# Optimization experiments

Measured on AMD Instinct MI355X. Metric: run time of the kernel, lower is better.

## Reference

```python
import jax, jax.numpy as jnp
import numpy as np

VOCAB = 1000
PAD_ID = 0
D = 256      # d_model
H = 256      # hidden_size
G = 4 * H    # LSTM gate width
B = 64
S = 256      # src_len
TGT = 257    # tgt_len (decode T = 256)


def setup_inputs() -> dict:
    key = jax.random.key(0)
    ks = iter(jax.random.split(key, 48))
    def p(shape, scale):
        return jax.random.normal(next(ks), shape, jnp.float32) * scale
    inp = {}
    inp['src'] = jax.random.randint(next(ks), (B, S), 1, VOCAB)    # no PAD tokens
    inp['tgt'] = jax.random.randint(next(ks), (B, TGT), 1, VOCAB)
    inp['emb'] = p((VOCAB, D), D ** -0.5).at[PAD_ID].set(0.0)       # padding_idx row zeroed
    s = 1.0 / np.sqrt(H)
    # encoder biLSTM: layer0 fwd/bwd (input D), layer1 fwd/bwd (input 2H)
    for name, din in [('e0f', D), ('e0b', D), ('e1f', 2 * H), ('e1b', 2 * H)]:
        inp[name + '_Wih'] = p((G, din), 1.0 / np.sqrt(din))
        inp[name + '_Whh'] = p((G, H), s)
        inp[name + '_bih'] = p((G,), s)
        inp[name + '_bhh'] = p((G,), s)
    # decoder LSTM: layer0 input D+2H, layer1 input H
    for name, din in [('d0', D + 2 * H), ('d1', H)]:
        inp[name + '_Wih'] = p((G, din), 1.0 / np.sqrt(din))
        inp[name + '_Whh'] = p((G, H), s)
        inp[name + '_bih'] = p((G,), s)
        inp[name + '_bhh'] = p((G,), s)
    inp['h_proj_W'] = p((H, 2 * H), 1.0 / np.sqrt(2 * H))
    inp['h_proj_b'] = p((H,), s)
    inp['c_proj_W'] = p((H, 2 * H), 1.0 / np.sqrt(2 * H))
    inp['c_proj_b'] = p((H,), s)
    inp['att_Wenc'] = p((H, 2 * H), 1.0 / np.sqrt(2 * H))
    inp['att_Wdec'] = p((H, H), s)
    inp['att_v'] = p((H,), s)
    return inp


def _cell(gates, c):
    # PyTorch gate order: i, f, g, o
    i, f, g, o = jnp.split(gates, 4, axis=-1)
    c = jax.nn.sigmoid(f) * c + jax.nn.sigmoid(i) * jnp.tanh(g)
    return jax.nn.sigmoid(o) * jnp.tanh(c), c


def _lstm(x, Wih, Whh, bih, bhh, reverse=False):
    # x: (B, S, din) -> outputs (B, S, H), final (h, c)
    Bsz = x.shape[0]
    Hd = Whh.shape[1]
    pre = jnp.swapaxes(x @ Wih.T + bih + bhh, 0, 1)  # (S, B, 4H)
    def step(carry, g):
        h, c = carry
        h, c = _cell(g + h @ Whh.T, c)
        return (h, c), h
    init = (jnp.zeros((Bsz, Hd), x.dtype), jnp.zeros((Bsz, Hd), x.dtype))
    (hT, cT), ys = jax.lax.scan(step, init, pre, reverse=reverse)
    return jnp.swapaxes(ys, 0, 1), hT, cT


def reference(src, tgt, emb,
              e0f_Wih, e0f_Whh, e0f_bih, e0f_bhh,
              e0b_Wih, e0b_Whh, e0b_bih, e0b_bhh,
              e1f_Wih, e1f_Whh, e1f_bih, e1f_bhh,
              e1b_Wih, e1b_Whh, e1b_bih, e1b_bhh,
              d0_Wih, d0_Whh, d0_bih, d0_bhh,
              d1_Wih, d1_Whh, d1_bih, d1_bhh,
              h_proj_W, h_proj_b, c_proj_W, c_proj_b,
              att_Wenc, att_Wdec, att_v):
    mask = (src == PAD_ID)                       # (B, S), all False here
    x0 = emb[src]                                # (B, S, D)
    # ---- bidirectional 2-layer encoder ----
    f0, _, _ = _lstm(x0, e0f_Wih, e0f_Whh, e0f_bih, e0f_bhh)
    b0, _, _ = _lstm(x0, e0b_Wih, e0b_Whh, e0b_bih, e0b_bhh, reverse=True)
    x1 = jnp.concatenate([f0, b0], axis=-1)      # (B, S, 2H)
    f1, hf, cf = _lstm(x1, e1f_Wih, e1f_Whh, e1f_bih, e1f_bhh)
    b1, hb, cb = _lstm(x1, e1b_Wih, e1b_Whh, e1b_bih, e1b_bhh, reverse=True)
    enc_out = jnp.concatenate([f1, b1], axis=-1)  # (B, S, 2H)
    # ---- decoder init (shared across both decoder layers) ----
    h0 = jnp.tanh(jnp.concatenate([hf, hb], -1) @ h_proj_W.T + h_proj_b)
    c0 = jnp.tanh(jnp.concatenate([cf, cb], -1) @ c_proj_W.T + c_proj_b)
    # ---- teacher-forced decode with Bahdanau attention ----
    enc_proj = enc_out @ att_Wenc.T              # (B, S, H), hoisted out of the loop
    tgt_emb = emb[tgt[:, :-1]]                   # (B, T, D)

    def dec_step(carry, xt):
        hl0, cl0, hl1, cl1 = carry
        energy = jnp.tanh(enc_proj + (hl1 @ att_Wdec.T)[:, None, :])  # (B, S, H)
        scores = energy @ att_v                                        # (B, S)
        scores = jnp.where(mask, -jnp.inf, scores)
        w = jax.nn.softmax(scores, axis=-1)
        ctx = jnp.einsum('bs,bse->be', w, enc_out)                     # (B, 2H)
        x = jnp.concatenate([xt, ctx], axis=-1)                        # (B, D+2H)
        hl0, cl0 = _cell(x @ d0_Wih.T + d0_bih + d0_bhh + hl0 @ d0_Whh.T, cl0)
        hl1, cl1 = _cell(hl0 @ d1_Wih.T + d1_bih + d1_bhh + hl1 @ d1_Whh.T, cl1)
        return (hl0, cl0, hl1, cl1), hl1

    _, outs = jax.lax.scan(dec_step, (h0, c0, h0, c0), jnp.swapaxes(tgt_emb, 0, 1))
    out = jnp.swapaxes(outs, 0, 1)               # (B, T, H); out_proj is None (H == D)
    return out @ emb.T                           # weight-tied fc_out -> (B, T, VOCAB)
```

## Files before the change

### kernel.cpp

```cpp
#include <hip/hip_runtime.h>
#include <hip/hip_bf16.h>
#include <stdint.h>

#define B_ 64
#define S_ 256
#define T_ 256
#define D_ 256
#define H_ 256
#define V_ 1000

__device__ __forceinline__ float blo(unsigned u){ return __uint_as_float(u << 16); }
__device__ __forceinline__ float bhi(unsigned u){ return __uint_as_float(u & 0xffff0000u); }
__device__ __forceinline__ float sigm(float x){ return 1.0f / (1.0f + __expf(-x)); }
__device__ __forceinline__ float tanhfast(float x){ float e = __expf(2.0f * x); return 1.0f - 2.0f / (e + 1.0f); }

__device__ __forceinline__ void cellupd(float a0, float a1, float a2, float a3, float& c, float& h){
  float cn = sigm(a1) * c + sigm(a0) * tanhfast(a2);
  c = cn;
  h = sigm(a3) * tanhfast(cn);
}

__device__ __forceinline__ float wredmax(float v){
  #pragma unroll
  for (int o = 32; o > 0; o >>= 1) v = fmaxf(v, __shfl_xor(v, o));
  return v;
}
__device__ __forceinline__ float wredsum(float v){
  #pragma unroll
  for (int o = 32; o > 0; o >>= 1) v += __shfl_xor(v, o);
  return v;
}

__device__ __forceinline__ void ast(float* p, float v){
  __hip_atomic_store(p, v, __ATOMIC_RELAXED, __HIP_MEMORY_SCOPE_AGENT);
}
__device__ __forceinline__ float ald(const float* p){
  return __hip_atomic_load(p, __ATOMIC_RELAXED, __HIP_MEMORY_SCOPE_AGENT);
}

__global__ void probe_kernel(const unsigned short* __restrict__ w, int* __restrict__ flag)
{
  int cnt = 0;
  for (int i = threadIdx.x; i < 4096; i += 64) {
    unsigned e = (w[i] >> 7) & 0xFFu;
    if (e >= 0xC0u) cnt++;
  }
  #pragma unroll
  for (int o = 32; o > 0; o >>= 1) cnt += __shfl_xor(cnt, o);
  if (threadIdx.x == 0) *flag = (cnt > 32) ? 1 : 0;
}

__device__ __forceinline__ float load_any(const void* src, int i, int isf32){
  return isf32 ? ((const float*)src)[i]
               : __uint_as_float(((unsigned)((const unsigned short*)src)[i]) << 16);
}

__global__ void conv_kernel(const void* __restrict__ src, float* __restrict__ dst, int n,
                            const int* __restrict__ flagp)
{
  int i = blockIdx.x * 256 + threadIdx.x;
  if (i >= n) return;
  dst[i] = load_any(src, i, *flagp);
}

__global__ void bias_kernel(const void* __restrict__ a, const void* __restrict__ bsrc,
                            float* __restrict__ dst, int n, const int* __restrict__ flagp)
{
  int i = blockIdx.x * 256 + threadIdx.x;
  if (i >= n) return;
  int f = *flagp;
  dst[i] = load_any(a, i, f) + load_any(bsrc, i, f);
}

__global__ void swzb_kernel(const void* __restrict__ src, unsigned short* __restrict__ dst,
                            int R, int Ks, int Kt, int c0, int perm, const int* __restrict__ flagp)
{
  int i = blockIdx.x * 256 + threadIdx.x;
  if (i >= R * Ks) return;
  int r = i / Ks;
  int k = i - r * Ks;
  int kk = k + c0;
  int Rr = r;
  if (perm) {
    int g = r >> 8, j = r & 255;
    Rr = ((j >> 4) << 6) + (g << 4) + (j & 15);
  }
  float v = load_any(src, i, *flagp);
  __hip_bfloat16 bv = __float2bfloat16(v);
  dst[(((size_t)(Rr >> 6) * (size_t)(Kt >> 3) + (size_t)(kk >> 3)) * 64 + (Rr & 63)) * 8 + (kk & 7)] =
      *(unsigned short*)&bv;
}

template<int K>
__device__ __forceinline__ float dot1w(const unsigned short* __restrict__ w, int r,
                                       const float* __restrict__ xs)
{
  constexpr int KC = K >> 3;
  const uint4* __restrict__ p = (const uint4*)w + (size_t)(r >> 6) * KC * 64 + (r & 63);
  float a = 0.0f;
  #pragma unroll 4
  for (int kc = 0; kc < KC; ++kc) {
    const uint4 q = p[(size_t)kc * 64];
    const float4 x0 = *(const float4*)(xs + kc * 8);
    const float4 x1 = *(const float4*)(xs + kc * 8 + 4);
    a += blo(q.x)*x0.x + bhi(q.x)*x0.y + blo(q.y)*x0.z + bhi(q.y)*x0.w
       + blo(q.z)*x1.x + bhi(q.z)*x1.y + blo(q.w)*x1.z + bhi(q.w)*x1.w;
  }
  return a;
}

template<int KC, int SL>
__device__ __forceinline__ void dot4s(const unsigned short* __restrict__ w, int j, int q,
                                      const float* __restrict__ xsl, float out4[4])
{
  const int lane = j & 63, wq = j >> 6;
  const uint4* __restrict__ p0 = (const uint4*)w + ((size_t)(wq     ) * KC + q * SL) * 64 + lane;
  const uint4* __restrict__ p1 = (const uint4*)w + ((size_t)(wq + 4 ) * KC + q * SL) * 64 + lane;
  const uint4* __restrict__ p2 = (const uint4*)w + ((size_t)(wq + 8 ) * KC + q * SL) * 64 + lane;
  const uint4* __restrict__ p3 = (const uint4*)w + ((size_t)(wq + 12) * KC + q * SL) * 64 + lane;
  float a0 = 0.0f, a1 = 0.0f, a2 = 0.0f, a3 = 0.0f;
  #pragma unroll 4
  for (int kc = 0; kc < SL; ++kc) {
    const float4 x0 = *(const float4*)(xsl + kc * 8);
    const float4 x1 = *(const float4*)(xsl + kc * 8 + 4);
    uint4 qq;
    qq = p0[(size_t)kc * 64];
    a0 += blo(qq.x)*x0.x + bhi(qq.x)*x0.y + blo(qq.y)*x0.z + bhi(qq.y)*x0.w
        + blo(qq.z)*x1.x + bhi(qq.z)*x1.y + blo(qq.w)*x1.z + bhi(qq.w)*x1.w;
    qq = p1[(size_t)kc * 64];
    a1 += blo(qq.x)*x0.x + bhi(qq.x)*x0.y + blo(qq.y)*x0.z + bhi(qq.y)*x0.w
        + blo(qq.z)*x1.x + bhi(qq.z)*x1.y + blo(qq.w)*x1.z + bhi(qq.w)*x1.w;
    qq = p2[(size_t)kc * 64];
    a2 += blo(qq.x)*x0.x + bhi(qq.x)*x0.y + blo(qq.y)*x0.z + bhi(qq.y)*x0.w
        + blo(qq.z)*x1.x + bhi(qq.z)*x1.y + blo(qq.w)*x1.z + bhi(qq.w)*x1.w;
    qq = p3[(size_t)kc * 64];
    a3 += blo(qq.x)*x0.x + bhi(qq.x)*x0.y + blo(qq.y)*x0.z + bhi(qq.y)*x0.w
        + blo(qq.z)*x1.x + bhi(qq.z)*x1.y + blo(qq.w)*x1.z + bhi(qq.w)*x1.w;
  }
  out4[0] = a0; out4[1] = a1; out4[2] = a2; out4[3] = a3;
}

__global__ __launch_bounds__(1024, 1) void enc0_kernel(
    const int* __restrict__ src, const float* __restrict__ emb_f,
    const unsigned short* __restrict__ wF, const unsigned short* __restrict__ wB,
    const float* __restrict__ bF, const float* __restrict__ bB,
    float* __restrict__ f0, float* __restrict__ b0)
{
  const int blk = blockIdx.x, dir = blk >> 6, b = blk & 63, tid = threadIdx.x;
  const unsigned short* w = dir ? wB : wF;
  const float* bi = dir ? bB : bF;
  float* outp = dir ? b0 : f0;
  __shared__ __align__(16) float xs[512];
  __shared__ __align__(16) float work4[4096];
  const int q = tid >> 8, j = tid & 255;
  float bias_g[4];
  if (tid < 256) {
    #pragma unroll
    for (int g = 0; g < 4; ++g) bias_g[g] = bi[g * 256 + tid];
    xs[256 + tid] = 0.0f;
  }
  float c = 0.0f, h = 0.0f;
  const size_t bS = (size_t)b * S_;
  for (int t = 0; t < S_; ++t) {
    const int tp = dir ? (S_ - 1 - t) : t;
    const int tok = src[bS + tp];
    if (tid < 256) xs[tid] = emb_f[(size_t)tok * D_ + tid];
    __syncthreads();
    float o4[4];
    dot4s<64, 16>(w, j, q, xs + q * 128, o4);
    #pragma unroll
    for (int g = 0; g < 4; ++g) work4[(g * 4 + q) * 256 + j] = o4[g];
    __syncthreads();
    if (tid < 256) {
      float gv[4];
      #pragma unroll
      for (int g = 0; g < 4; ++g)
        gv[g] = work4[(g*4+0)*256 + tid] + work4[(g*4+1)*256 + tid]
              + work4[(g*4+2)*256 + tid] + work4[(g*4+3)*256 + tid] + bias_g[g];
      cellupd(gv[0], gv[1], gv[2], gv[3], c, h);
      xs[256 + tid] = h;
      outp[(bS + tp) * H_ + tid] = h;
    }
    __syncthreads();
  }
}

__global__ __launch_bounds__(1024, 1) void enc1_kernel(
    const float* __restrict__ f0, const float* __restrict__ b0,
    const unsigned short* __restrict__ wF, const unsigned short* __restrict__ wB,
    const float* __restrict__ bF, const float* __restrict__ bB,
    float* __restrict__ enc_out, float* __restrict__ hcbuf)
{
  const int blk = blockIdx.x, dir = blk >> 6, b = blk & 63, tid = threadIdx.x;
  const unsigned short* w = dir ? wB : wF;
  const float* bi = dir ? bB : bF;
  __shared__ __align__(16) float xs[768];
  __shared__ __align__(16) float work4[4096];
  const int q = tid >> 8, j = tid & 255;
  float bias_g[4];
  if (tid < 256) {
    #pragma unroll
    for (int g = 0; g < 4; ++g) bias_g[g] = bi[g * 256 + tid];
    xs[512 + tid] = 0.0f;
  }
  float c = 0.0f, h = 0.0f;
  const size_t bS = (size_t)b * S_;
  for (int t = 0; t < S_; ++t) {
    const int tp = dir ? (S_ - 1 - t) : t;
    const size_t row = (bS + tp) * (size_t)H_;
    if (tid < 512) {
      const int jj = tid & 255;
      xs[tid] = (tid < 256) ? f0[row + jj] : b0[row + jj];
    }
    __syncthreads();
    float o4[4];
    dot4s<96, 24>(w, j, q, xs + q * 192, o4);
    #pragma unroll
    for (int g = 0; g < 4; ++g) work4[(g * 4 + q) * 256 + j] = o4[g];
    __syncthreads();
    if (tid < 256) {
      float gv[4];
      #pragma unroll
      for (int g = 0; g < 4; ++g)
        gv[g] = work4[(g*4+0)*256 + tid] + work4[(g*4+1)*256 + tid]
              + work4[(g*4+2)*256 + tid] + work4[(g*4+3)*256 + tid] + bias_g[g];
      cellupd(gv[0], gv[1], gv[2], gv[3], c, h);
      xs[512 + tid] = h;
      enc_out[(bS + tp) * 512 + dir * 256 + tid] = h;
    }
    __syncthreads();
  }
  if (tid < 256) {
    const int BH = B_ * H_;
    float* hout = hcbuf + (dir ? 2 * BH : 0);
    hout[(size_t)b * H_ + tid]      = h;
    hout[BH + (size_t)b * H_ + tid] = c;
  }
}

__global__ __launch_bounds__(256) void proj_kernel(
    const float* __restrict__ enc_out, const float* __restrict__ hcbuf,
    const unsigned short* __restrict__ wenc_s,
    const unsigned short* __restrict__ hpw_s, const unsigned short* __restrict__ cpw_s,
    const float* __restrict__ hpb_f, const float* __restrict__ cpb_f,
    float* __restrict__ epT, float* __restrict__ h0c0)
{
  __shared__ __align__(16) float xs[16 * 512];
  const int blk = blockIdx.x, tid = threadIdx.x;
  if (blk < 1024) {
    const int b = blk >> 4, s0 = (blk & 15) * 16;
    const float* srcp = enc_out + ((size_t)b * S_ + s0) * 512;
    for (int i = tid; i < 16 * 512; i += 256) xs[i] = srcp[i];
    __syncthreads();
    float acc[16];
    #pragma unroll
    for (int r = 0; r < 16; ++r) acc[r] = 0.0f;
    const uint4* p = (const uint4*)wenc_s + (size_t)(tid >> 6) * 64 * 64 + (tid & 63);
    for (int kc = 0; kc < 64; ++kc) {
      const uint4 q = p[(size_t)kc * 64];
      const float w0=blo(q.x), w1=bhi(q.x), w2=blo(q.y), w3=bhi(q.y),
                  w4=blo(q.z), w5=bhi(q.z), w6=blo(q.w), w7=bhi(q.w);
      #pragma unroll
      for (int r = 0; r < 16; ++r) {
        const float4 x0 = *(const float4*)(xs + r * 512 + kc * 8);
        const float4 x1 = *(const float4*)(xs + r * 512 + kc * 8 + 4);
        acc[r] += w0*x0.x + w1*x0.y + w2*x0.z + w3*x0.w + w4*x1.x + w5*x1.y + w6*x1.z + w7*x1.w;
      }
    }
    float* dst = epT + ((size_t)b * S_ + (size_t)tid) * 256 + s0;
    #pragma unroll
    for (int r = 0; r < 16; ++r) dst[r] = acc[r];
  } else {
    const int b = blk - 1024;
    const int BH = B_ * H_;
    xs[tid]        = hcbuf[(size_t)b * H_ + tid];
    xs[256 + tid]  = hcbuf[2 * BH + (size_t)b * H_ + tid];
    xs[512 + tid]  = hcbuf[BH + (size_t)b * H_ + tid];
    xs[768 + tid]  = hcbuf[3 * BH + (size_t)b * H_ + tid];
    __syncthreads();
    const float hv = dot1w<512>(hpw_s, tid, xs)       + hpb_f[tid];
    const float cv = dot1w<512>(cpw_s, tid, xs + 512) + cpb_f[tid];
    h0c0[(size_t)b * H_ + tid]              = tanhfast(hv);
    h0c0[(size_t)BH + (size_t)b * H_ + tid] = tanhfast(cv);
  }
}

__global__ __launch_bounds__(256) void gemb_kernel(
    const float* __restrict__ emb_f, const unsigned short* __restrict__ d0p,
    float* __restrict__ gemb)
{
  __shared__ __align__(16) float xs[16 * 256];
  const int blk = blockIdx.x, tg = blk >> 2, cg = blk & 3, tid = threadIdx.x;
  for (int i = tid; i < 16 * 256; i += 256) {
    const int tk = tg * 16 + (i >> 8);
    xs[i] = (tk < V_) ? emb_f[(size_t)tk * 256 + (i & 255)] : 0.0f;
  }
  __syncthreads();
  const int r = cg * 256 + tid;
  const uint4* p = (const uint4*)d0p + (size_t)(r >> 6) * 128 * 64 + (r & 63);
  float acc[16];
  #pragma unroll
  for (int ti = 0; ti < 16; ++ti) acc[ti] = 0.0f;
  for (int kc = 0; kc < 32; ++kc) {
    const uint4 q = p[(size_t)kc * 64];
    const float w0=blo(q.x), w1=bhi(q.x), w2=blo(q.y), w3=bhi(q.y),
                w4=blo(q.z), w5=bhi(q.z), w6=blo(q.w), w7=bhi(q.w);
    #pragma unroll
    for (int ti = 0; ti < 16; ++ti) {
      const float4 x0 = *(const float4*)(xs + ti * 256 + kc * 8);
      const float4 x1 = *(const float4*)(xs + ti * 256 + kc * 8 + 4);
      acc[ti] += w0*x0.x + w1*x0.y + w2*x0.z + w3*x0.w + w4*x1.x + w5*x1.y + w6*x1.z + w7*x1.w;
    }
  }
  #pragma unroll
  for (int ti = 0; ti < 16; ++ti) {
    const int tk = tg * 16 + ti;
    if (tk < V_) gemb[(size_t)tk * 1024 + r] = acc[ti];
  }
}

__global__ void zero_cnt_kernel(int* __restrict__ cnt)
{
  cnt[threadIdx.x] = 0;
}

__global__ __launch_bounds__(1024, 1) void dec_fused_kernel(
    const int* __restrict__ src, const int* __restrict__ tgt,
    const float* __restrict__ h0c0,
    const float* __restrict__ epT, const float* __restrict__ enc_out,
    const float* __restrict__ gemb,
    const unsigned short* __restrict__ wdec_s,
    const unsigned short* __restrict__ d0p, const unsigned short* __restrict__ d1p,
    const float* __restrict__ d0b, const float* __restrict__ d1b,
    const float* __restrict__ attv_f,
    float* __restrict__ dec_h,
    float* __restrict__ esc, float* __restrict__ ctxg,
    float* __restrict__ hl0g, float* __restrict__ hl1g,
    int* __restrict__ cnt)
{
  const int Bk = blockIdx.x, b = Bk & 63, k = Bk >> 6, tid = threadIdx.x;
  const int j64 = k * 64;

  __shared__ __align__(16) float epl[64 * 260];
  __shared__ __align__(16) unsigned short eol[128 * 264];
  __shared__ __align__(16) float work[1024];
  __shared__ __align__(16) float xs0[768];
  __shared__ __align__(16) float hl1s[256];
  __shared__ __align__(16) float hl0n[256];
  __shared__ __align__(16) float qarr[256];
  __shared__ __align__(16) float vv[256];
  __shared__ __align__(16) float msk[256];
  __shared__ __align__(16) float wsm[256];
  __shared__ __align__(16) float cl0s[64];
  __shared__ __align__(16) float cl1s[64];
  __shared__ float red[16];

  const float* epb = epT + (size_t)b * (S_ * 256);
  const float* eob = enc_out + (size_t)b * (S_ * 512);

  for (int i = tid; i < 64 * 256; i += 1024) {
    const int si = i & 63, j = i >> 6;
    epl[si * 260 + j] = epb[(size_t)j * 256 + j64 + si];
  }
  for (int i = tid; i < 128 * 256; i += 1024) {
    const int dl = i & 127, s = i >> 7;
    __hip_bfloat16 bv = __float2bfloat16(eob[(size_t)s * 512 + k * 128 + dl]);
    eol[dl * 264 + s] = *(unsigned short*)&bv;
  }
  if (tid < 256) {
    vv[tid]  = attv_f[tid];
    msk[tid] = (src[b * 256 + tid] == 0) ? -1e30f : 0.0f;
    const float h0 = h0c0[b * 256 + tid];
    hl1s[tid] = h0;
    xs0[512 + tid] = h0;
  }
  if (tid < 64) {
    const float c0 = h0c0[B_ * H_ + b * 256 + j64 + tid];
    cl0s[tid] = c0; cl1s[tid] = c0;
  }
  __syncthreads();

  int syncno = 0;
#define GSYNC() do {                                                                    \
    ++syncno;                                                                           \
    __syncthreads();    \
    if (tid == 0) {                                                                     \
      __hip_atomic_fetch_add(&cnt[b], 1, __ATOMIC_RELAXED, __HIP_MEMORY_SCOPE_AGENT);   \
      while (__hip_atomic_load(&cnt[b], __ATOMIC_RELAXED, __HIP_MEMORY_SCOPE_AGENT)     \
             < 4 * syncno)                                                              \
        __builtin_amdgcn_s_sleep(2);                                                    \
    }                                                                                   \
    __syncthreads();                                                                    \
    asm volatile("" ::: "memory");                                                      \
  } while (0)

  for (int t = 0; t < T_; ++t) {
    {
      const int j = tid & 255, q4 = tid >> 8;
      const uint4* p = (const uint4*)wdec_s + ((size_t)(j >> 6) * 32 + q4 * 8) * 64 + (j & 63);
      const float* xsl = hl1s + q4 * 64;
      float a = 0.0f;
      #pragma unroll
      for (int kc = 0; kc < 8; ++kc) {
        const uint4 w = p[(size_t)kc * 64];
        const float4 x0 = *(const float4*)(xsl + kc * 8);
        const float4 x1 = *(const float4*)(xsl + kc * 8 + 4);
        a += blo(w.x)*x0.x + bhi(w.x)*x0.y + blo(w.y)*x0.z + bhi(w.y)*x0.w
           + blo(w.z)*x1.x + bhi(w.z)*x1.y + blo(w.w)*x1.z + bhi(w.w)*x1.w;
      }
      work[q4 * 256 + j] = a;
    }
    __syncthreads();
    if (tid < 256)
      qarr[tid] = work[tid] + work[256 + tid] + work[512 + tid] + work[768 + tid];
    __syncthreads();

    {
      const int si = tid & 63, jg = tid >> 6;
      const float* ep = epl + si * 260 + jg * 16;
      const float* qv = qarr + jg * 16;
      const float* vp = vv + jg * 16;
      float a = 0.0f;
      #pragma unroll
      for (int i = 0; i < 16; ++i)
        a += vp[i] * tanhfast(ep[i] + qv[i]);
      work[jg * 64 + si] = a;
    }
    __syncthreads();
    if (tid < 64) {
      float e = 0.0f;
      #pragma unroll
      for (int g = 0; g < 16; ++g) e += work[g * 64 + tid];
      ast(&esc[b * 256 + j64 + tid], e + msk[j64 + tid]);
    }
    GSYNC();

    {
      const float e = (tid < 256) ? ald(&esc[b * 256 + tid]) : -1e30f;
      const float m0 = wredmax(e);
      if (tid < 256 && (tid & 63) == 0) red[tid >> 6] = m0;
      __syncthreads();
      const float m = fmaxf(fmaxf(red[0], red[1]), fmaxf(red[2], red[3]));
      const float pe = (tid < 256) ? __expf(e - m) : 0.0f;
      const float ss = wredsum(pe);
      if (tid < 256 && (tid & 63) == 0) red[4 + (tid >> 6)] = ss;
      __syncthreads();
      const float inv = 1.0f / ((red[4] + red[5]) + (red[6] + red[7]));
      if (tid < 256) wsm[tid] = pe * inv;
    }
    __syncthreads();

    {
      const int dq = tid & 127, sg = tid >> 7;
      const uint4* er = (const uint4*)(eol + dq * 264 + sg * 32);
      const float* wp = wsm + sg * 32;
      float a = 0.0f;
      #pragma unroll
      for (int i4 = 0; i4 < 4; ++i4) {
        const uint4 q = er[i4];
        const float* w8 = wp + i4 * 8;
        a += blo(q.x)*w8[0] + bhi(q.x)*w8[1] + blo(q.y)*w8[2] + bhi(q.y)*w8[3]
           + blo(q.z)*w8[4] + bhi(q.z)*w8[5] + blo(q.w)*w8[6] + bhi(q.w)*w8[7];
      }
      work[sg * 128 + dq] = a;
    }
    __syncthreads();
    if (tid < 128) {
      float a = 0.0f;
      #pragma unroll
      for (int g = 0; g < 8; ++g) a += work[g * 128 + tid];
      ast(&ctxg[b * 512 + k * 128 + tid], a);
    }
    GSYNC();
    if (tid < 512) xs0[tid] = ald(&ctxg[b * 512 + tid]);
    __syncthreads();

    {
      const int lr = tid & 255, q4 = tid >> 8;
      const int g = lr >> 6, jj = lr & 63;
      const uint4* p = (const uint4*)d0p + ((size_t)(g * 4 + k) * 128 + 32 + q4 * 24) * 64 + jj;
      const float* xsl = xs0 + q4 * 192;
      float a = 0.0f;
      #pragma unroll 4
      for (int kc = 0; kc < 24; ++kc) {
        const uint4 w = p[(size_t)kc * 64];
        const float4 x0 = *(const float4*)(xsl + kc * 8);
        const float4 x1 = *(const float4*)(xsl + kc * 8 + 4);
        a += blo(w.x)*x0.x + bhi(w.x)*x0.y + blo(w.y)*x0.z + bhi(w.y)*x0.w
           + blo(w.z)*x1.x + bhi(w.z)*x1.y + blo(w.w)*x1.z + bhi(w.w)*x1.w;
      }
      work[q4 * 256 + lr] = a;
    }
    __syncthreads();
    if (tid < 64) {
      const int tok = tgt[b * 257 + t];
      const float* ge = gemb + (size_t)tok * 1024;
      float gv[4];
      #pragma unroll
      for (int g = 0; g < 4; ++g) {
        const int lr = g * 64 + tid;
        gv[g] = work[lr] + work[256 + lr] + work[512 + lr] + work[768 + lr]
              + d0b[g * 256 + j64 + tid] + ge[g * 256 + j64 + tid];
      }
      float c = cl0s[tid], h;
      cellupd(gv[0], gv[1], gv[2], gv[3], c, h);
      cl0s[tid] = c;
      ast(&hl0g[b * 256 + j64 + tid], h);
    }
    GSYNC();
    if (tid < 256) {
      const float hv = ald(&hl0g[b * 256 + tid]);
      hl0n[tid] = hv;
      xs0[512 + tid] = hv;
    }
    __syncthreads();

    {
      const int lr = tid & 255, q4 = tid >> 8;
      const int g = lr >> 6, jj = lr & 63;
      const uint4* p = (const uint4*)d1p + ((size_t)(g * 4 + k) * 64 + q4 * 16) * 64 + jj;
      const float* xsl = (q4 < 2) ? (hl0n + q4 * 128) : (hl1s + (q4 - 2) * 128);
      float a = 0.0f;
      #pragma unroll 4
      for (int kc = 0; kc < 16; ++kc) {
        const uint4 w = p[(size_t)kc * 64];
        const float4 x0 = *(const float4*)(xsl + kc * 8);
        const float4 x1 = *(const float4*)(xsl + kc * 8 + 4);
        a += blo(w.x)*x0.x + bhi(w.x)*x0.y + blo(w.y)*x0.z + bhi(w.y)*x0.w
           + blo(w.z)*x1.x + bhi(w.z)*x1.y + blo(w.w)*x1.z + bhi(w.w)*x1.w;
      }
      work[q4 * 256 + lr] = a;
    }
    __syncthreads();
    if (tid < 64) {
      float gv[4];
      #pragma unroll
      for (int g = 0; g < 4; ++g) {
        const int lr = g * 64 + tid;
        gv[g] = work[lr] + work[256 + lr] + work[512 + lr] + work[768 + lr]
              + d1b[g * 256 + j64 + tid];
      }
      float c = cl1s[tid], h;
      cellupd(gv[0], gv[1], gv[2], gv[3], c, h);
      cl1s[tid] = c;
      ast(&hl1g[b * 256 + j64 + tid], h);
      dec_h[((size_t)b * T_ + t) * H_ + j64 + tid] = h;
    }
    GSYNC();
    if (tid < 256) hl1s[tid] = ald(&hl1g[b * 256 + tid]);
    __syncthreads();
  }
#undef GSYNC
}

__global__ __launch_bounds__(256) void out_kernel(
    const float* __restrict__ dec_h, const unsigned short* __restrict__ emb_s,
    void* __restrict__ out, const int* __restrict__ flagp)
{
  __shared__ __align__(16) float hs[16 * 256];
  const int blk = blockIdx.x, tid = threadIdx.x;
  const int isf32 = *flagp;
  const float* srcp = dec_h + (size_t)blk * (16 * 256);
  for (int i = tid; i < 16 * 256; i += 256) hs[i] = srcp[i];
  __syncthreads();
  #pragma unroll
  for (int vi = 0; vi < 4; ++vi) {
    const int v = tid + vi * 256;
    if (v < V_) {
      const uint4* p = (const uint4*)emb_s + (size_t)(v >> 6) * 32 * 64 + (v & 63);
      float acc[16];
      #pragma unroll
      for (int r = 0; r < 16; ++r) acc[r] = 0.0f;
      for (int kc = 0; kc < 32; ++kc) {
        const uint4 q = p[(size_t)kc * 64];
        const float w0=blo(q.x), w1=bhi(q.x), w2=blo(q.y), w3=bhi(q.y),
                    w4=blo(q.z), w5=bhi(q.z), w6=blo(q.w), w7=bhi(q.w);
        #pragma unroll
        for (int r = 0; r < 16; ++r) {
          const float4 x0 = *(const float4*)(hs + r * 256 + kc * 8);
          const float4 x1 = *(const float4*)(hs + r * 256 + kc * 8 + 4);
          acc[r] += w0*x0.x + w1*x0.y + w2*x0.z + w3*x0.w + w4*x1.x + w5*x1.y + w6*x1.z + w7*x1.w;
        }
      }
      const size_t rowbase = (size_t)blk * 16;
      if (isf32) {
        float* o = (float*)out;
        #pragma unroll
        for (int r = 0; r < 16; ++r) o[(rowbase + r) * V_ + v] = acc[r];
      } else {
        __hip_bfloat16* o = (__hip_bfloat16*)out;
        #pragma unroll
        for (int r = 0; r < 16; ++r) o[(rowbase + r) * V_ + v] = __float2bfloat16(acc[r]);
      }
    }
  }
}

extern "C" void kernel_launch(void* const* d_in, const int* in_sizes, int n_in,
                              void* d_out, int out_size, void* d_ws, size_t ws_size,
                              hipStream_t stream)
{
  (void)in_sizes; (void)n_in; (void)out_size; (void)ws_size;
  const int* src = (const int*)d_in[0];
  const int* tgt = (const int*)d_in[1];

  char* base = (char*)d_ws;
  int* flag = (int*)base;
  float* ws = (float*)(base + 256);
  size_t off = 0;
  float* f0      = ws + off; off += (size_t)B_ * S_ * H_;
  float* b0      = ws + off; off += (size_t)B_ * S_ * H_;
  float* enc_out = ws + off; off += (size_t)B_ * S_ * 2 * H_;
  float* hcbuf   = ws + off; off += 4 * (size_t)B_ * H_;
  float* h0c0    = ws + off; off += 2 * (size_t)B_ * H_;
  float* emb_f   = ws + off; off += (size_t)V_ * D_;
  float* gemb    = ws + off; off += (size_t)V_ * 1024;
  float* esc     = ws + off; off += (size_t)B_ * S_;
  float* ctxg    = ws + off; off += (size_t)B_ * 512;
  float* hl0g    = ws + off; off += (size_t)B_ * H_;
  float* hl1g    = ws + off; off += (size_t)B_ * H_;
  int*   cntp    = (int*)(ws + off); off += 64;
  float* e0f_b   = ws + off; off += 1024;
  float* e0b_b   = ws + off; off += 1024;
  float* e1f_b   = ws + off; off += 1024;
  float* e1b_b   = ws + off; off += 1024;
  float* d0_b    = ws + off; off += 1024;
  float* d1_b    = ws + off; off += 1024;
  float* hpb_f   = ws + off; off += 256;
  float* cpb_f   = ws + off; off += 256;
  float* attv_f  = ws + off; off += 256;
  unsigned short* us = (unsigned short*)(ws + off);
  size_t uo = 0;
  unsigned short* e0f_s  = us + uo; uo += (size_t)1024 * 512;
  unsigned short* e0b_s  = us + uo; uo += (size_t)1024 * 512;
  unsigned short* e1f_s  = us + uo; uo += (size_t)1024 * 768;
  unsigned short* e1b_s  = us + uo; uo += (size_t)1024 * 768;
  unsigned short* d0p_s  = us + uo; uo += (size_t)1024 * 1024;
  unsigned short* d1p_s  = us + uo; uo += (size_t)1024 * 512;
  unsigned short* wdec_s = us + uo; uo += (size_t)256 * 256;
  unsigned short* wenc_s = us + uo; uo += (size_t)256 * 512;
  unsigned short* hpw_s  = us + uo; uo += (size_t)256 * 512;
  unsigned short* cpw_s  = us + uo; uo += (size_t)256 * 512;
  unsigned short* emb_s  = us + uo; uo += (size_t)1024 * 256;
  float* dec_h = f0;
  float* epT   = b0;

  hipLaunchKernelGGL(probe_kernel, dim3(1), dim3(64), 0, stream,
                     (const unsigned short*)d_in[3], flag);

  auto swz = [&](int idx, unsigned short* dst, int R, int Ks, int Kt, int c0, int perm){
    const int n = R * Ks;
    hipLaunchKernelGGL(swzb_kernel, dim3((n + 255) / 256), dim3(256), 0, stream,
                       d_in[idx], dst, R, Ks, Kt, c0, perm, flag);
  };
  auto bias2 = [&](int ia, int ib, float* dst, int n){
    hipLaunchKernelGGL(bias_kernel, dim3((n + 255) / 256), dim3(256), 0, stream,
                       d_in[ia], d_in[ib], dst, n, flag);
  };

  hipLaunchKernelGGL(conv_kernel, dim3((V_ * D_ + 255) / 256), dim3(256), 0, stream,
                     d_in[2], emb_f, V_ * D_, flag);
  hipLaunchKernelGGL(conv_kernel, dim3(1), dim3(256), 0, stream, d_in[28], hpb_f, 256, flag);
  hipLaunchKernelGGL(conv_kernel, dim3(1), dim3(256), 0, stream, d_in[30], cpb_f, 256, flag);
  hipLaunchKernelGGL(conv_kernel, dim3(1), dim3(256), 0, stream, d_in[33], attv_f, 256, flag);
  bias2(5, 6, e0f_b, 1024);   bias2(9, 10, e0b_b, 1024);
  bias2(13, 14, e1f_b, 1024); bias2(17, 18, e1b_b, 1024);
  bias2(21, 22, d0_b, 1024);  bias2(25, 26, d1_b, 1024);
  swz(3,  e0f_s, 1024, 256, 512, 0, 0);   swz(4,  e0f_s, 1024, 256, 512, 256, 0);
  swz(7,  e0b_s, 1024, 256, 512, 0, 0);   swz(8,  e0b_s, 1024, 256, 512, 256, 0);
  swz(11, e1f_s, 1024, 512, 768, 0, 0);   swz(12, e1f_s, 1024, 256, 768, 512, 0);
  swz(15, e1b_s, 1024, 512, 768, 0, 0);   swz(16, e1b_s, 1024, 256, 768, 512, 0);
  swz(19, d0p_s, 1024, 768, 1024, 0, 0);  swz(20, d0p_s, 1024, 256, 1024, 768, 0);
  swz(23, d1p_s, 1024, 256, 512, 0, 0);   swz(24, d1p_s, 1024, 256, 512, 256, 0);
  swz(32, wdec_s, 256, 256, 256, 0, 0);
  swz(31, wenc_s, 256, 512, 512, 0, 0);
  swz(27, hpw_s, 256, 512, 512, 0, 0);
  swz(29, cpw_s, 256, 512, 512, 0, 0);
  swz(2,  emb_s, 1000, 256, 256, 0, 0);

  hipLaunchKernelGGL(gemb_kernel, dim3(252), dim3(256), 0, stream, emb_f, d0p_s, gemb);

  hipLaunchKernelGGL(enc0_kernel, dim3(128), dim3(1024), 0, stream,
                     src, emb_f, e0f_s, e0b_s, e0f_b, e0b_b, f0, b0);
  hipLaunchKernelGGL(enc1_kernel, dim3(128), dim3(1024), 0, stream,
                     f0, b0, e1f_s, e1b_s, e1f_b, e1b_b, enc_out, hcbuf);
  hipLaunchKernelGGL(proj_kernel, dim3(1088), dim3(256), 0, stream,
                     enc_out, hcbuf, wenc_s, hpw_s, cpw_s, hpb_f, cpb_f, epT, h0c0);

  hipLaunchKernelGGL(zero_cnt_kernel, dim3(1), dim3(64), 0, stream, cntp);

  {
    const int* srcp_ = src; const int* tgtp_ = tgt;
    const float* h0c0_ = h0c0; const float* epT_ = epT; const float* eo_ = enc_out;
    const float* gemb_ = gemb;
    const unsigned short* wdec_ = wdec_s;
    const unsigned short* d0p_ = d0p_s; const unsigned short* d1p_ = d1p_s;
    const float* d0b_ = d0_b; const float* d1b_ = d1_b; const float* attv_ = attv_f;
    float* dech_ = dec_h; float* esc_ = esc; float* ctxg_ = ctxg;
    float* hl0g_ = hl0g; float* hl1g_ = hl1g; int* cnt_ = cntp;
    void* kargs[] = {
      (void*)&srcp_, (void*)&tgtp_, (void*)&h0c0_, (void*)&epT_, (void*)&eo_,
      (void*)&gemb_, (void*)&wdec_, (void*)&d0p_, (void*)&d1p_,
      (void*)&d0b_, (void*)&d1b_, (void*)&attv_,
      (void*)&dech_, (void*)&esc_, (void*)&ctxg_, (void*)&hl0g_, (void*)&hl1g_, (void*)&cnt_
    };
    hipError_t e = hipLaunchCooperativeKernel((const void*)dec_fused_kernel,
                                              dim3(256), dim3(1024), kargs, 0, stream);
    if (e != hipSuccess) {
      hipLaunchKernelGGL(dec_fused_kernel, dim3(256), dim3(1024), 0, stream,
                         srcp_, tgtp_, h0c0_, epT_, eo_, gemb_, wdec_, d0p_, d1p_,
                         d0b_, d1b_, attv_, dech_, esc_, ctxg_, hl0g_, hl1g_, cnt_);
    }
  }

  hipLaunchKernelGGL(out_kernel, dim3(1024), dim3(256), 0, stream,
                     dec_h, emb_s, d_out, flag);
}
```

Baseline: 15.05 ms.

## Repartition attention scoring across hidden dim and colocate batch blocks

Each of the four blocks per batch now computes partial attention energies over all 256 source positions for its own 64-wide slice of the hidden dimension, rather than the full hidden dimension for 64 source positions. Each block therefore computes only its 64 query entries instead of recomputing all 256. The four partial energy vectors are summed after the global sync, and the esc buffer grows fourfold to hold them. The change also maps the four blocks of a batch to adjacent block IDs, hoists bias and embedding-gate loads into registers before the GEMVs, and raises unroll factors. The aim is to cut redundant query-projection work and latency per step, at the cost of more global reads in the softmax stage.

```diff
diff --git a/kernel.cpp b/kernel.cpp
--- a/kernel.cpp
+++ b/kernel.cpp
@@ -338,17 +338,17 @@
     float* __restrict__ hl0g, float* __restrict__ hl1g,
     int* __restrict__ cnt)
 {
-  const int Bk = blockIdx.x, b = Bk & 63, k = Bk >> 6, tid = threadIdx.x;
+  const int Bk = blockIdx.x, b = Bk >> 2, k = Bk & 3, tid = threadIdx.x;
   const int j64 = k * 64;
 
-  __shared__ __align__(16) float epl[64 * 260];
+  __shared__ __align__(16) float epl[256 * 65];
   __shared__ __align__(16) unsigned short eol[128 * 264];
   __shared__ __align__(16) float work[1024];
   __shared__ __align__(16) float xs0[768];
   __shared__ __align__(16) float hl1s[256];
   __shared__ __align__(16) float hl0n[256];
-  __shared__ __align__(16) float qarr[256];
-  __shared__ __align__(16) float vv[256];
+  __shared__ __align__(16) float qloc[64];
+  __shared__ __align__(16) float vv[64];
   __shared__ __align__(16) float msk[256];
   __shared__ __align__(16) float wsm[256];
   __shared__ __align__(16) float cl0s[64];
@@ -358,9 +358,9 @@
   const float* epb = epT + (size_t)b * (S_ * 256);
   const float* eob = enc_out + (size_t)b * (S_ * 512);
 
-  for (int i = tid; i < 64 * 256; i += 1024) {
-    const int si = i & 63, j = i >> 6;
-    epl[si * 260 + j] = epb[(size_t)j * 256 + j64 + si];
+  for (int i = tid; i < 256 * 64; i += 1024) {
+    const int s = i & 255, jj = i >> 8;
+    epl[s * 65 + jj] = epb[(size_t)(j64 + jj) * 256 + s];
   }
   for (int i = tid; i < 128 * 256; i += 1024) {
     const int dl = i & 127, s = i >> 7;
@@ -368,15 +368,21 @@
     eol[dl * 264 + s] = *(unsigned short*)&bv;
   }
   if (tid < 256) {
-    vv[tid]  = attv_f[tid];
     msk[tid] = (src[b * 256 + tid] == 0) ? -1e30f : 0.0f;
     const float h0 = h0c0[b * 256 + tid];
     hl1s[tid] = h0;
     xs0[512 + tid] = h0;
   }
+  float b0r[4], b1r[4];
   if (tid < 64) {
+    vv[tid] = attv_f[j64 + tid];
     const float c0 = h0c0[B_ * H_ + b * 256 + j64 + tid];
     cl0s[tid] = c0; cl1s[tid] = c0;
+    #pragma unroll
+    for (int g = 0; g < 4; ++g) {
+      b0r[g] = d0b[g * 256 + j64 + tid];
+      b1r[g] = d1b[g * 256 + j64 + tid];
+    }
   }
   __syncthreads();
 
@@ -395,48 +401,62 @@
   } while (0)
 
   for (int t = 0; t < T_; ++t) {
+    float gpre[4];
+    if (tid < 64) {
+      const float* ge = gemb + (size_t)tgt[b * 257 + t] * 1024;
+      #pragma unroll
+      for (int g = 0; g < 4; ++g) gpre[g] = ge[g * 256 + j64 + tid];
+    }
+
     {
-      const int j = tid & 255, q4 = tid >> 8;
-      const uint4* p = (const uint4*)wdec_s + ((size_t)(j >> 6) * 32 + q4 * 8) * 64 + (j & 63);
-      const float* xsl = hl1s + q4 * 64;
-      float a = 0.0f;
-      #pragma unroll
-      for (int kc = 0; kc < 8; ++kc) {
-        const uint4 w = p[(size_t)kc * 64];
-        const float4 x0 = *(const float4*)(xsl + kc * 8);
-        const float4 x1 = *(const float4*)(xsl + kc * 8 + 4);
-        a += blo(w.x)*x0.x + bhi(w.x)*x0.y + blo(w.y)*x0.z + bhi(w.y)*x0.w
-           + blo(w.z)*x1.x + bhi(w.z)*x1.y + blo(w.w)*x1.z + bhi(w.w)*x1.w;
-      }
-      work[q4 * 256 + j] = a;
-    }
-    __syncthreads();
-    if (tid < 256)
-      qarr[tid] = work[tid] + work[256 + tid] + work[512 + tid] + work[768 + tid];
+      const int jj = tid & 63, q16 = tid >> 6;
+      const uint4* p = (const uint4*)wdec_s + ((size_t)k * 32 + q16 * 2) * 64 + jj;
+      const float* xsl = hl1s + q16 * 16;
+      const uint4 w0 = p[0], w1 = p[64];
+      const float4 xa = *(const float4*)(xsl);
+      const float4 xb = *(const float4*)(xsl + 4);
+      const float4 xc = *(const float4*)(xsl + 8);
+      const float4 xd = *(const float4*)(xsl + 12);
+      const float a =
+          blo(w0.x)*xa.x + bhi(w0.x)*xa.y + blo(w0.y)*xa.z + bhi(w0.y)*xa.w
+        + blo(w0.z)*xb.x + bhi(w0.z)*xb.y + blo(w0.w)*xb.z + bhi(w0.w)*xb.w
+        + blo(w1.x)*xc.x + bhi(w1.x)*xc.y + blo(w1.y)*xc.z + bhi(w1.y)*xc.w
+        + blo(w1.z)*xd.x + bhi(w1.z)*xd.y + blo(w1.w)*xd.z + bhi(w1.w)*xd.w;
+      work[q16 * 64 + jj] = a;
+    }
+    __syncthreads();
+    if (tid < 64) {
+      float q = 0.0f;
+      #pragma unroll
+      for (int i = 0; i < 16; ++i) q += work[i * 64 + tid];
+      qloc[tid] = q;
+    }
     __syncthreads();
 
     {
-      const int si = tid & 63, jg = tid >> 6;
-      const float* ep = epl + si * 260 + jg * 16;
-      const float* qv = qarr + jg * 16;
-      const float* vp = vv + jg * 16;
+      const int s = tid & 255, jq = tid >> 8;
+      const float* ep = epl + s * 65 + jq * 16;
+      const float* qv = qloc + jq * 16;
+      const float* vp = vv + jq * 16;
       float a = 0.0f;
       #pragma unroll
       for (int i = 0; i < 16; ++i)
         a += vp[i] * tanhfast(ep[i] + qv[i]);
-      work[jg * 64 + si] = a;
-    }
-    __syncthreads();
-    if (tid < 64) {
-      float e = 0.0f;
-      #pragma unroll
-      for (int g = 0; g < 16; ++g) e += work[g * 64 + tid];
-      ast(&esc[b * 256 + j64 + tid], e + msk[j64 + tid]);
-    }
+      work[jq * 256 + s] = a;
+    }
+    __syncthreads();
+    if (tid < 256)
+      ast(&esc[b * 1024 + k * 256 + tid],
+          work[tid] + work[256 + tid] + work[512 + tid] + work[768 + tid]);
     GSYNC();
 
     {
-      const float e = (tid < 256) ? ald(&esc[b * 256 + tid]) : -1e30f;
+      float e = -1e30f;
+      if (tid < 256) {
+        const float* eb = esc + b * 1024;
+        e = ald(&eb[tid]) + ald(&eb[256 + tid]) + ald(&eb[512 + tid]) + ald(&eb[768 + tid])
+          + msk[tid];
+      }
       const float m0 = wredmax(e);
       if (tid < 256 && (tid & 63) == 0) red[tid >> 6] = m0;
       __syncthreads();
@@ -481,7 +501,7 @@
       const uint4* p = (const uint4*)d0p + ((size_t)(g * 4 + k) * 128 + 32 + q4 * 24) * 64 + jj;
       const float* xsl = xs0 + q4 * 192;
       float a = 0.0f;
-      #pragma unroll 4
+      #pragma unroll 8
       for (int kc = 0; kc < 24; ++kc) {
         const uint4 w = p[(size_t)kc * 64];
         const float4 x0 = *(const float4*)(xsl + kc * 8);
@@ -493,14 +513,12 @@
     }
     __syncthreads();
     if (tid < 64) {
-      const int tok = tgt[b * 257 + t];
-      const float* ge = gemb + (size_t)tok * 1024;
       float gv[4];
       #pragma unroll
       for (int g = 0; g < 4; ++g) {
         const int lr = g * 64 + tid;
         gv[g] = work[lr] + work[256 + lr] + work[512 + lr] + work[768 + lr]
-              + d0b[g * 256 + j64 + tid] + ge[g * 256 + j64 + tid];
+              + b0r[g] + gpre[g];
       }
       float c = cl0s[tid], h;
       cellupd(gv[0], gv[1], gv[2], gv[3], c, h);
@@ -521,7 +539,7 @@
       const uint4* p = (const uint4*)d1p + ((size_t)(g * 4 + k) * 64 + q4 * 16) * 64 + jj;
       const float* xsl = (q4 < 2) ? (hl0n + q4 * 128) : (hl1s + (q4 - 2) * 128);
       float a = 0.0f;
-      #pragma unroll 4
+      #pragma unroll 8
       for (int kc = 0; kc < 16; ++kc) {
         const uint4 w = p[(size_t)kc * 64];
         const float4 x0 = *(const float4*)(xsl + kc * 8);
@@ -537,8 +555,7 @@
       #pragma unroll
       for (int g = 0; g < 4; ++g) {
         const int lr = g * 64 + tid;
-        gv[g] = work[lr] + work[256 + lr] + work[512 + lr] + work[768 + lr]
-              + d1b[g * 256 + j64 + tid];
+        gv[g] = work[lr] + work[256 + lr] + work[512 + lr] + work[768 + lr] + b1r[g];
       }
       float c = cl1s[tid], h;
       cellupd(gv[0], gv[1], gv[2], gv[3], c, h);
@@ -615,7 +632,7 @@
   float* h0c0    = ws + off; off += 2 * (size_t)B_ * H_;
   float* emb_f   = ws + off; off += (size_t)V_ * D_;
   float* gemb    = ws + off; off += (size_t)V_ * 1024;
-  float* esc     = ws + off; off += (size_t)B_ * S_;
+  float* esc     = ws + off; off += (size_t)B_ * S_ * 4;
   float* ctxg    = ws + off; off += (size_t)B_ * 512;
   float* hl0g    = ws + off; off += (size_t)B_ * H_;
   float* hl1g    = ws + off; off += (size_t)B_ * H_;
```

Measured after the change: 17.69 ms. 1.18x slower.
